# Kernel optimization log

Hardware: AMD Instinct MI355X
Metric: run time of the kernel (lower is better)

The kernel has to match this reference:

```python
import jax, jax.numpy as jnp
import numpy as np

BETA = 0.25

def _encoder(x, W0, b0, W1, b1, W2, b2):
    # MLP: Linear+ReLU, Linear+ReLU, Linear (dims 768->512->256->64)
    h = jax.nn.relu(x @ W0 + b0)
    h = jax.nn.relu(h @ W1 + b1)
    return h @ W2 + b2

def _rvq(z, codebooks):
    # Residual vector quantization over L=4 levels (structurally distinct loop).
    residual = z
    x_q = jnp.zeros_like(z)
    losses = []
    codes = []
    for l in range(codebooks.shape[0]):
        cb = codebooks[l]  # [K, e]
        # squared L2 distances [N, K] via expansion (avoids materializing [N,K,e])
        d = (jnp.sum(residual * residual, axis=1, keepdims=True)
             - 2.0 * residual @ cb.T
             + jnp.sum(cb * cb, axis=1))
        idx = jnp.argmin(d, axis=1)           # [N]
        q = cb[idx]                            # gather [N, e]
        # codebook loss + beta * commitment loss
        loss = (jnp.mean((jax.lax.stop_gradient(q) - residual) ** 2)
                + BETA * jnp.mean((q - jax.lax.stop_gradient(residual)) ** 2))
        losses.append(loss)
        # straight-through estimator
        q_st = residual + jax.lax.stop_gradient(q - residual)
        residual = residual - q_st
        x_q = x_q + q_st
        codes.append(idx)
    rq_loss = jnp.mean(jnp.stack(losses))
    return x_q, rq_loss, jnp.stack(codes)  # codes: [L, N] int


def setup_inputs() -> dict:
    key = jax.random.key(0)
    ks = jax.random.split(key, 8)
    N, D = 131072, 768
    dims = [768, 512, 256, 64]
    x = jax.random.normal(ks[0], (N, D), dtype=jnp.float32)
    W0 = jax.random.normal(ks[1], (dims[0], dims[1]), dtype=jnp.float32) * (1.0 / np.sqrt(dims[0]))
    b0 = jnp.zeros((dims[1],), dtype=jnp.float32)
    W1 = jax.random.normal(ks[2], (dims[1], dims[2]), dtype=jnp.float32) * (1.0 / np.sqrt(dims[1]))
    b1 = jnp.zeros((dims[2],), dtype=jnp.float32)
    W2 = jax.random.normal(ks[3], (dims[2], dims[3]), dtype=jnp.float32) * (1.0 / np.sqrt(dims[2]))
    b2 = jnp.zeros((dims[3],), dtype=jnp.float32)
    codebooks = jax.random.normal(ks[4], (4, 256, 64), dtype=jnp.float32)
    return {"x": x, "W0": W0, "b0": b0, "W1": W1, "b1": b1, "W2": W2, "b2": b2,
            "codebooks": codebooks}


def reference(x, W0, b0, W1, b1, W2, b2, codebooks):
    z = _encoder(x, W0, b0, W1, b1, W2, b2)          # [N, 64]
    x_q, rq_loss, codes = _rvq(z, codebooks)
    return x_q, rq_loss, codes
```

## Files before the change

kernel.cpp:

```cpp
#include <hip/hip_runtime.h>
#include <hip/hip_bf16.h>


typedef double d2v __attribute__((ext_vector_type(2)));

#define GBM 128
#define GBN 64
#define GBK 16
#define GTM 8
#define GTN 4

template<bool RELU>
__global__ __launch_bounds__(256) void gemm_bias(
    const float* __restrict__ A, const float* __restrict__ W,
    const float* __restrict__ bias, float* __restrict__ C,
    int M, int N, int K)
{
    __shared__ float As[GBK][GBM + 4];
    __shared__ float Bs[GBK][GBN + 4];

    const int tid = threadIdx.x;
    const int tx = tid & 15;
    const int ty = tid >> 4;
    const int col0 = blockIdx.x * GBN;
    const int row0 = blockIdx.y * GBM;

    const float* Ab = A + (size_t)row0 * K;
    const float* Wb = W + col0;

    float acc[GTM][GTN] = {};

    for (int k0 = 0; k0 < K; k0 += GBK) {
#pragma unroll
        for (int i = 0; i < 2; ++i) {
            int pos = tid + i * 256;
            int m  = pos >> 2;
            int k4 = (pos & 3) * 4;
            float4 v = *reinterpret_cast<const float4*>(Ab + (size_t)m * K + k0 + k4);
            As[k4 + 0][m] = v.x; As[k4 + 1][m] = v.y;
            As[k4 + 2][m] = v.z; As[k4 + 3][m] = v.w;
        }
        {
            int kk = tid >> 4;
            int n4 = (tid & 15) * 4;
            float4 v = *reinterpret_cast<const float4*>(Wb + (size_t)(k0 + kk) * N + n4);
            *reinterpret_cast<float4*>(&Bs[kk][n4]) = v;
        }
        __syncthreads();
#pragma unroll
        for (int kk = 0; kk < GBK; ++kk) {
            float4 a0 = *reinterpret_cast<const float4*>(&As[kk][ty * GTM]);
            float4 a1 = *reinterpret_cast<const float4*>(&As[kk][ty * GTM + 4]);
            float4 bv = *reinterpret_cast<const float4*>(&Bs[kk][tx * GTN]);
            float a[GTM] = {a0.x, a0.y, a0.z, a0.w, a1.x, a1.y, a1.z, a1.w};
            float b[GTN] = {bv.x, bv.y, bv.z, bv.w};
#pragma unroll
            for (int m = 0; m < GTM; ++m)
#pragma unroll
                for (int n = 0; n < GTN; ++n)
                    acc[m][n] = fmaf(a[m], b[n], acc[m][n]);
        }
        __syncthreads();
    }

    float bv[GTN];
#pragma unroll
    for (int n = 0; n < GTN; ++n) bv[n] = bias[col0 + tx * GTN + n];
#pragma unroll
    for (int m = 0; m < GTM; ++m) {
        int row = row0 + ty * GTM + m;
        float4 o;
        float v0 = acc[m][0] + bv[0];
        float v1 = acc[m][1] + bv[1];
        float v2 = acc[m][2] + bv[2];
        float v3 = acc[m][3] + bv[3];
        if (RELU) {
            v0 = fmaxf(v0, 0.f); v1 = fmaxf(v1, 0.f);
            v2 = fmaxf(v2, 0.f); v3 = fmaxf(v3, 0.f);
        }
        o.x = v0; o.y = v1; o.z = v2; o.w = v3;
        *reinterpret_cast<float4*>(C + (size_t)row * N + col0 + tx * GTN) = o;
    }
}

__global__ void cb_norms(const float* __restrict__ cb,
                         double* __restrict__ cn64, float* __restrict__ cnf) {
    int c = blockIdx.x * 64 + threadIdx.x;
    const float* p = cb + (size_t)c * 64;
    double s = 0.0;
#pragma unroll
    for (int j = 0; j < 64; ++j) {
        double v = (double)p[j];
        s = fma(v, v, s);
    }
    cn64[c] = s;
    cnf[c]  = (float)s;
}

__global__ void build_cbw(const float* __restrict__ cb, double* __restrict__ cbw) {
    int i = blockIdx.x * 256 + threadIdx.x;
    cbw[i] = -2.0 * (double)cb[i];
}

#define EGUARD 1e-3

__device__ __forceinline__ double rank64(const double* __restrict__ p,
                                         double R0, const float (&rd)[64]) {
    double c0 = 0.0, c1 = 0.0, c2 = 0.0, c3 = 0.0;
#pragma unroll
    for (int j = 0; j < 16; ++j) {
        d2v x = *reinterpret_cast<const d2v*>(p + j * 4);
        d2v y = *reinterpret_cast<const d2v*>(p + j * 4 + 2);
        c0 = fma(x[0], (double)rd[j * 4 + 0], c0);
        c1 = fma(x[1], (double)rd[j * 4 + 1], c1);
        c2 = fma(y[0], (double)rd[j * 4 + 2], c2);
        c3 = fma(y[1], (double)rd[j * 4 + 3], c3);
    }
    return R0 + ((c0 + c1) + (c2 + c3));
}

__global__ __launch_bounds__(256, 2) void rvq_v5(
    const float* __restrict__ z,
    const float* __restrict__ cbf,
    const double* __restrict__ cbw,
    const double* __restrict__ cn64,
    const float* __restrict__ cnf,
    float* __restrict__ xq,
    float* __restrict__ codes,
    double* __restrict__ partials,
    int row0, int Ntot)
{
    __shared__ float sd1[4][64];
    __shared__ float sd2[4][64];
    __shared__ int   si1[4][64];
    __shared__ int   si2[4][64];

    const int tid  = threadIdx.x;
    const int lane = tid & 63;
    const int w    = tid >> 6;
    const int wu   = __builtin_amdgcn_readfirstlane(w);
    const int blk  = blockIdx.x;
    const int grow0 = row0 + blk * 64;

    float rd[64];
    const float* zr = z + (size_t)(blk * 64 + lane) * 64;
#pragma unroll
    for (int q = 0; q < 16; ++q) {
        float4 v = *reinterpret_cast<const float4*>(zr + q * 4);
        rd[q * 4 + 0] = v.x; rd[q * 4 + 1] = v.y;
        rd[q * 4 + 2] = v.z; rd[q * 4 + 3] = v.w;
    }

    double sse = 0.0;

    for (int lv = 0; lv < 4; ++lv) {
        const int cbase = lv * 256;
        __syncthreads();

        const float* cwl = cbf + (size_t)(cbase + wu * 64) * 64;
        const float* cnl = cnf + cbase + wu * 64;

        float d1 = 3.4e38f, d2 = 3.4e38f;
        int   i1 = 0,       i2 = 0;

#pragma unroll 1
        for (int c = 0; c < 64; ++c) {
            const float* cp = cwl + c * 64;
            float acc8[8];
#pragma unroll
            for (int q = 0; q < 8; ++q) {
                float4 va = *reinterpret_cast<const float4*>(cp + q * 8);
                float4 vb = *reinterpret_cast<const float4*>(cp + q * 8 + 4);
                float t = 0.f;
                t = fmaf(va.x, rd[q * 8 + 0], t);
                t = fmaf(va.y, rd[q * 8 + 1], t);
                t = fmaf(va.z, rd[q * 8 + 2], t);
                t = fmaf(va.w, rd[q * 8 + 3], t);
                t = fmaf(vb.x, rd[q * 8 + 4], t);
                t = fmaf(vb.y, rd[q * 8 + 5], t);
                t = fmaf(vb.z, rd[q * 8 + 6], t);
                t = fmaf(vb.w, rd[q * 8 + 7], t);
                acc8[q] = t;
            }
            float dot = ((acc8[0] + acc8[1]) + (acc8[2] + acc8[3]))
                      + ((acc8[4] + acc8[5]) + (acc8[6] + acc8[7]));
            float d = fmaf(-2.f, dot, cnl[c]);
            int code = wu * 64 + c;
            if (d < d1) { d2 = d1; i2 = i1; d1 = d; i1 = code; }
            else if (d < d2) { d2 = d; i2 = code; }
        }

        sd1[w][lane] = d1; si1[w][lane] = i1;
        sd2[w][lane] = d2; si2[w][lane] = i2;
        __syncthreads();

        float bd1 = sd1[0][lane]; int bi1 = si1[0][lane]; int wstar = 0;
#pragma unroll
        for (int ww = 1; ww < 4; ++ww) {
            float dd = sd1[ww][lane]; int ii = si1[ww][lane];
            if (dd < bd1 || (dd == bd1 && ii < bi1)) { bd1 = dd; bi1 = ii; wstar = ww; }
        }
        float d2g = 3.4e38f; int i2g = 0;
#pragma unroll
        for (int ww = 0; ww < 4; ++ww) {
            float dd = (ww == wstar) ? sd2[ww][lane] : sd1[ww][lane];
            int   ii = (ww == wstar) ? si2[ww][lane] : si1[ww][lane];
            if (dd < d2g) { d2g = dd; i2g = ii; }
        }

        double R1 = rank64(cbw + (size_t)(cbase + bi1) * 64, cn64[cbase + bi1], rd);
        double R2 = rank64(cbw + (size_t)(cbase + i2g) * 64, cn64[cbase + i2g], rd);
        int ci; double Rw;
        if (R1 < R2 || (R1 == R2 && bi1 < i2g)) { ci = bi1; Rw = R1; }
        else                                    { ci = i2g; Rw = R2; }

        if (!(Rw < (double)d2g - EGUARD)) {
            float l8f = fminf(fminf(sd2[0][lane], sd2[1][lane]),
                              fminf(sd2[2][lane], sd2[3][lane]));
            double L8 = (double)l8f;
            double Rm = 1.0e300; int im = 0;
#pragma unroll
            for (int ww = 0; ww < 4; ++ww) {
#pragma unroll
                for (int k = 0; k < 2; ++k) {
                    int cc = k ? si2[ww][lane] : si1[ww][lane];
                    double R = rank64(cbw + (size_t)(cbase + cc) * 64,
                                      cn64[cbase + cc], rd);
                    if (R < Rm || (R == Rm && cc < im)) { Rm = R; im = cc; }
                }
            }
            if (Rm < L8 - EGUARD) {
                ci = im;
            } else {
                double dmin = 1.0e300; int imin = 0;
#pragma unroll 1
                for (int c = 0; c < 256; ++c) {
                    double R = rank64(cbw + (size_t)(cbase + c) * 64,
                                      cn64[cbase + c], rd);
                    if (R < dmin) { dmin = R; imin = c; }
                }
                ci = imin;
            }
        }

        const float* qp = cbf + (size_t)(cbase + ci) * 64;
        double lsse = 0.0;
#pragma unroll
        for (int q = 0; q < 16; ++q) {
            float4 qv = *reinterpret_cast<const float4*>(qp + q * 4);
            float r0 = rd[q * 4 + 0], r1 = rd[q * 4 + 1];
            float r2 = rd[q * 4 + 2], r3 = rd[q * 4 + 3];
            if (w == 0) {
                float e0 = qv.x - r0, e1 = qv.y - r1;
                float e2 = qv.z - r2, e3 = qv.w - r3;
                lsse = fma((double)e0, (double)e0, lsse);
                lsse = fma((double)e1, (double)e1, lsse);
                lsse = fma((double)e2, (double)e2, lsse);
                lsse = fma((double)e3, (double)e3, lsse);
            }
            rd[q * 4 + 0] = r0 - qv.x; rd[q * 4 + 1] = r1 - qv.y;
            rd[q * 4 + 2] = r2 - qv.z; rd[q * 4 + 3] = r3 - qv.w;
        }
        if (w == 0) {
            sse += lsse;
            codes[(size_t)lv * Ntot + grow0 + lane] = (float)ci;
        }
    }

    if (w == 0) {
        size_t base = (size_t)(grow0 + lane) * 64;
#pragma unroll
        for (int q = 0; q < 16; ++q) {
            float4 zv = *reinterpret_cast<const float4*>(zr + q * 4);
            float4 o;
            o.x = zv.x - rd[q * 4 + 0];
            o.y = zv.y - rd[q * 4 + 1];
            o.z = zv.z - rd[q * 4 + 2];
            o.w = zv.w - rd[q * 4 + 3];
            *reinterpret_cast<float4*>(xq + base + q * 4) = o;
        }
        double s = sse;
#pragma unroll
        for (int off = 32; off > 0; off >>= 1) {
            union { double d; int i[2]; } u; u.d = s;
            u.i[0] = __shfl_down(u.i[0], off, 64);
            u.i[1] = __shfl_down(u.i[1], off, 64);
            s += u.d;
        }
        if (lane == 0) partials[grow0 >> 6] = s;
    }
}

__global__ void loss_final(const double* __restrict__ partials, int n,
                           float* __restrict__ out, double scale) {
    __shared__ double s[256];
    double acc = 0.0;
    for (int i = threadIdx.x; i < n; i += 256) acc += partials[i];
    s[threadIdx.x] = acc;
    __syncthreads();
    for (int off = 128; off > 0; off >>= 1) {
        if ((int)threadIdx.x < off) s[threadIdx.x] += s[threadIdx.x + off];
        __syncthreads();
    }
    if (threadIdx.x == 0) *out = (float)(s[0] * scale);
}

extern "C" void kernel_launch(void* const* d_in, const int* in_sizes, int n_in,
                              void* d_out, int out_size, void* d_ws, size_t ws_size,
                              hipStream_t stream) {
    const float* x  = (const float*)d_in[0];
    const float* W0 = (const float*)d_in[1];
    const float* b0 = (const float*)d_in[2];
    const float* W1 = (const float*)d_in[3];
    const float* b1 = (const float*)d_in[4];
    const float* W2 = (const float*)d_in[5];
    const float* b2 = (const float*)d_in[6];
    const float* cb = (const float*)d_in[7];

    const int N = in_sizes[0] / 768;

    float* out   = (float*)d_out;
    float* xq    = out;
    float* loss  = out + (size_t)N * 64;
    float* codes = loss + 1;

    const int nblk_total = N / 64;
    const size_t tail_floats = 131072 + 2048 + 2 * (size_t)nblk_total + 1024 + 64;

    size_t avail = ws_size / 4;
    avail = (avail > tail_floats) ? (avail - tail_floats) : 0;
    int Nc = (int)(avail / 832);
    Nc = (Nc / 128) * 128;
    if (Nc > N) Nc = N;
    if (Nc < 128) Nc = 128;

    float* ws = (float*)d_ws;
    float* h0 = ws;
    float* h1 = h0 + (size_t)Nc * 512;
    float* z  = h1 + (size_t)Nc * 256;
    double* cbw      = (double*)(ws + (size_t)Nc * 832);
    double* cn64     = cbw + 65536;
    double* partials = cn64 + 1024;
    float*  cnf      = (float*)(partials + nblk_total);

    cb_norms <<<16, 64, 0, stream>>>(cb, cn64, cnf);
    build_cbw<<<256, 256, 0, stream>>>(cb, cbw);

    for (int r0 = 0; r0 < N; r0 += Nc) {
        int cur = (N - r0 < Nc) ? (N - r0) : Nc;
        gemm_bias<true ><<<dim3(512 / GBN, cur / GBM), 256, 0, stream>>>(
            x + (size_t)r0 * 768, W0, b0, h0, cur, 512, 768);
        gemm_bias<true ><<<dim3(256 / GBN, cur / GBM), 256, 0, stream>>>(
            h0, W1, b1, h1, cur, 256, 512);
        gemm_bias<false><<<dim3( 64 / GBN, cur / GBM), 256, 0, stream>>>(
            h1, W2, b2, z, cur, 64, 256);
        rvq_v5<<<cur / 64, 256, 0, stream>>>(
            z, cb, cbw, cn64, cnf, xq, codes, partials, r0, N);
    }

    loss_final<<<1, 256, 0, stream>>>(partials, nblk_total, loss,
                                      1.25 / (4.0 * (double)N * 64.0));
}
```

Before: 2.823 ms.

## Use 128x128 register-blocked GEMM with prefetch for first two encoder layers

Adds a gemm128 kernel that computes a 128x128 output tile per block, with each thread holding an 8x8 accumulator. It prefetches the next K-slice into registers while computing the current one (software pipelining). The first two encoder layers switch to this kernel, and the last layer keeps the old 128x64 kernel with its macros inlined. The goal is higher arithmetic intensity and less LDS and global traffic per FMA, plus latency hiding, at the cost of more registers and possibly lower occupancy.

```diff
diff --git a/kernel.cpp b/kernel.cpp
--- a/kernel.cpp
+++ b/kernel.cpp
@@ -4,11 +4,110 @@
 
 typedef double d2v __attribute__((ext_vector_type(2)));
 
-#define GBM 128
-#define GBN 64
-#define GBK 16
-#define GTM 8
-#define GTN 4
+template<bool RELU>
+__global__ __launch_bounds__(256) void gemm128(
+    const float* __restrict__ A, const float* __restrict__ W,
+    const float* __restrict__ bias, float* __restrict__ C,
+    int M, int N, int K)
+{
+    __shared__ float As[16][132];
+    __shared__ float Bs[16][132];
+
+    const int tid = threadIdx.x;
+    const int tx = tid & 15;
+    const int ty = tid >> 4;
+    const int col0 = blockIdx.x * 128;
+    const int row0 = blockIdx.y * 128;
+
+    const float* Ab = A + (size_t)row0 * K;
+    const float* Wb = W + col0;
+
+    const int am0 = tid >> 2,          ak0 = (tid & 3) * 4;
+    const int am1 = (tid + 256) >> 2,  ak1 = ((tid + 256) & 3) * 4;
+    const int bk0 = tid >> 5,          bn0 = (tid & 31) * 4;
+    const int bk1 = (tid + 256) >> 5,  bn1 = ((tid + 256) & 31) * 4;
+
+    float acc[8][8] = {};
+
+    float4 sa0 = *reinterpret_cast<const float4*>(Ab + (size_t)am0 * K + ak0);
+    float4 sa1 = *reinterpret_cast<const float4*>(Ab + (size_t)am1 * K + ak1);
+    float4 sb0 = *reinterpret_cast<const float4*>(Wb + (size_t)bk0 * N + bn0);
+    float4 sb1 = *reinterpret_cast<const float4*>(Wb + (size_t)bk1 * N + bn1);
+    As[ak0 + 0][am0] = sa0.x; As[ak0 + 1][am0] = sa0.y;
+    As[ak0 + 2][am0] = sa0.z; As[ak0 + 3][am0] = sa0.w;
+    As[ak1 + 0][am1] = sa1.x; As[ak1 + 1][am1] = sa1.y;
+    As[ak1 + 2][am1] = sa1.z; As[ak1 + 3][am1] = sa1.w;
+    *reinterpret_cast<float4*>(&Bs[bk0][bn0]) = sb0;
+    *reinterpret_cast<float4*>(&Bs[bk1][bn1]) = sb1;
+    __syncthreads();
+
+    for (int k0 = 0; k0 < K; k0 += 16) {
+        const bool hasNext = (k0 + 16 < K);
+        if (hasNext) {
+            const float* An = Ab + k0 + 16;
+            const float* Wn = Wb + (size_t)(k0 + 16) * N;
+            sa0 = *reinterpret_cast<const float4*>(An + (size_t)am0 * K + ak0);
+            sa1 = *reinterpret_cast<const float4*>(An + (size_t)am1 * K + ak1);
+            sb0 = *reinterpret_cast<const float4*>(Wn + (size_t)bk0 * N + bn0);
+            sb1 = *reinterpret_cast<const float4*>(Wn + (size_t)bk1 * N + bn1);
+        }
+
+#pragma unroll
+        for (int kk = 0; kk < 16; ++kk) {
+            float4 a0 = *reinterpret_cast<const float4*>(&As[kk][ty * 4]);
+            float4 a1 = *reinterpret_cast<const float4*>(&As[kk][64 + ty * 4]);
+            float4 b0 = *reinterpret_cast<const float4*>(&Bs[kk][tx * 4]);
+            float4 b1 = *reinterpret_cast<const float4*>(&Bs[kk][64 + tx * 4]);
+            float ar[8] = {a0.x, a0.y, a0.z, a0.w, a1.x, a1.y, a1.z, a1.w};
+            float br[8] = {b0.x, b0.y, b0.z, b0.w, b1.x, b1.y, b1.z, b1.w};
+#pragma unroll
+            for (int m = 0; m < 8; ++m)
+#pragma unroll
+                for (int n = 0; n < 8; ++n)
+                    acc[m][n] = fmaf(ar[m], br[n], acc[m][n]);
+        }
+
+        if (hasNext) {
+            __syncthreads();
+            As[ak0 + 0][am0] = sa0.x; As[ak0 + 1][am0] = sa0.y;
+            As[ak0 + 2][am0] = sa0.z; As[ak0 + 3][am0] = sa0.w;
+            As[ak1 + 0][am1] = sa1.x; As[ak1 + 1][am1] = sa1.y;
+            As[ak1 + 2][am1] = sa1.z; As[ak1 + 3][am1] = sa1.w;
+            *reinterpret_cast<float4*>(&Bs[bk0][bn0]) = sb0;
+            *reinterpret_cast<float4*>(&Bs[bk1][bn1]) = sb1;
+            __syncthreads();
+        }
+    }
+
+    float bl[4], bh[4];
+#pragma unroll
+    for (int n = 0; n < 4; ++n) {
+        bl[n] = bias[col0 + tx * 4 + n];
+        bh[n] = bias[col0 + 64 + tx * 4 + n];
+    }
+#pragma unroll
+    for (int half = 0; half < 2; ++half) {
+#pragma unroll
+        for (int r = 0; r < 4; ++r) {
+            int m = half * 4 + r;
+            int row = row0 + half * 64 + ty * 4 + r;
+            float4 lo, hi;
+            lo.x = acc[m][0] + bl[0]; lo.y = acc[m][1] + bl[1];
+            lo.z = acc[m][2] + bl[2]; lo.w = acc[m][3] + bl[3];
+            hi.x = acc[m][4] + bh[0]; hi.y = acc[m][5] + bh[1];
+            hi.z = acc[m][6] + bh[2]; hi.w = acc[m][7] + bh[3];
+            if (RELU) {
+                lo.x = fmaxf(lo.x, 0.f); lo.y = fmaxf(lo.y, 0.f);
+                lo.z = fmaxf(lo.z, 0.f); lo.w = fmaxf(lo.w, 0.f);
+                hi.x = fmaxf(hi.x, 0.f); hi.y = fmaxf(hi.y, 0.f);
+                hi.z = fmaxf(hi.z, 0.f); hi.w = fmaxf(hi.w, 0.f);
+            }
+            float* Cr = C + (size_t)row * N + col0;
+            *reinterpret_cast<float4*>(Cr + tx * 4) = lo;
+            *reinterpret_cast<float4*>(Cr + 64 + tx * 4) = hi;
+        }
+    }
+}
 
 template<bool RELU>
 __global__ __launch_bounds__(256) void gemm_bias(
@@ -16,21 +115,21 @@
     const float* __restrict__ bias, float* __restrict__ C,
     int M, int N, int K)
 {
-    __shared__ float As[GBK][GBM + 4];
-    __shared__ float Bs[GBK][GBN + 4];
+    __shared__ float As[16][132];
+    __shared__ float Bs[16][68];
 
     const int tid = threadIdx.x;
     const int tx = tid & 15;
     const int ty = tid >> 4;
-    const int col0 = blockIdx.x * GBN;
-    const int row0 = blockIdx.y * GBM;
+    const int col0 = blockIdx.x * 64;
+    const int row0 = blockIdx.y * 128;
 
     const float* Ab = A + (size_t)row0 * K;
     const float* Wb = W + col0;
 
-    float acc[GTM][GTN] = {};
-
-    for (int k0 = 0; k0 < K; k0 += GBK) {
+    float acc[8][4] = {};
+
+    for (int k0 = 0; k0 < K; k0 += 16) {
 #pragma unroll
         for (int i = 0; i < 2; ++i) {
             int pos = tid + i * 256;
@@ -48,27 +147,27 @@
         }
         __syncthreads();
 #pragma unroll
-        for (int kk = 0; kk < GBK; ++kk) {
-            float4 a0 = *reinterpret_cast<const float4*>(&As[kk][ty * GTM]);
-            float4 a1 = *reinterpret_cast<const float4*>(&As[kk][ty * GTM + 4]);
-            float4 bv = *reinterpret_cast<const float4*>(&Bs[kk][tx * GTN]);
-            float a[GTM] = {a0.x, a0.y, a0.z, a0.w, a1.x, a1.y, a1.z, a1.w};
-            float b[GTN] = {bv.x, bv.y, bv.z, bv.w};
-#pragma unroll
-            for (int m = 0; m < GTM; ++m)
-#pragma unroll
-                for (int n = 0; n < GTN; ++n)
+        for (int kk = 0; kk < 16; ++kk) {
+            float4 a0 = *reinterpret_cast<const float4*>(&As[kk][ty * 8]);
+            float4 a1 = *reinterpret_cast<const float4*>(&As[kk][ty * 8 + 4]);
+            float4 bv = *reinterpret_cast<const float4*>(&Bs[kk][tx * 4]);
+            float a[8] = {a0.x, a0.y, a0.z, a0.w, a1.x, a1.y, a1.z, a1.w};
+            float b[4] = {bv.x, bv.y, bv.z, bv.w};
+#pragma unroll
+            for (int m = 0; m < 8; ++m)
+#pragma unroll
+                for (int n = 0; n < 4; ++n)
                     acc[m][n] = fmaf(a[m], b[n], acc[m][n]);
         }
         __syncthreads();
     }
 
-    float bv[GTN];
-#pragma unroll
-    for (int n = 0; n < GTN; ++n) bv[n] = bias[col0 + tx * GTN + n];
-#pragma unroll
-    for (int m = 0; m < GTM; ++m) {
-        int row = row0 + ty * GTM + m;
+    float bv[4];
+#pragma unroll
+    for (int n = 0; n < 4; ++n) bv[n] = bias[col0 + tx * 4 + n];
+#pragma unroll
+    for (int m = 0; m < 8; ++m) {
+        int row = row0 + ty * 8 + m;
         float4 o;
         float v0 = acc[m][0] + bv[0];
         float v1 = acc[m][1] + bv[1];
@@ -79,7 +178,7 @@
             v2 = fmaxf(v2, 0.f); v3 = fmaxf(v3, 0.f);
         }
         o.x = v0; o.y = v1; o.z = v2; o.w = v3;
-        *reinterpret_cast<float4*>(C + (size_t)row * N + col0 + tx * GTN) = o;
+        *reinterpret_cast<float4*>(C + (size_t)row * N + col0 + tx * 4) = o;
     }
 }
 
@@ -348,11 +447,11 @@
 
     for (int r0 = 0; r0 < N; r0 += Nc) {
         int cur = (N - r0 < Nc) ? (N - r0) : Nc;
-        gemm_bias<true ><<<dim3(512 / GBN, cur / GBM), 256, 0, stream>>>(
+        gemm128<true ><<<dim3(512 / 128, cur / 128), 256, 0, stream>>>(
             x + (size_t)r0 * 768, W0, b0, h0, cur, 512, 768);
-        gemm_bias<true ><<<dim3(256 / GBN, cur / GBM), 256, 0, stream>>>(
+        gemm128<true ><<<dim3(256 / 128, cur / 128), 256, 0, stream>>>(
             h0, W1, b1, h1, cur, 256, 512);
-        gemm_bias<false><<<dim3( 64 / GBN, cur / GBM), 256, 0, stream>>>(
+        gemm_bias<false><<<dim3(1, cur / 128), 256, 0, stream>>>(
             h1, W2, b2, z, cur, 64, 256);
         rvq_v5<<<cur / 64, 256, 0, stream>>>(
             z, cb, cbw, cn64, cnf, xq, codes, partials, r0, N);
```

Result: faster. 2.668 ms (-5.5%).
